# Kernel tuning notes

Hardware: AMD Instinct MI355X
Metric: run time of the kernel (lower is better)

## Reference

```python
import jax, jax.numpy as jnp
import numpy as np

V, E, H = 50000, 300, 512
T, BIO, BIO_E = 9, 10, 64
REL_E, R = 128, 50
B, L = 16, 128


def _lstm(x, wih, whh, bih, bhh):
    # x: [B, L, E]; PyTorch gate order i, f, g, o
    h0 = jnp.zeros((x.shape[0], whh.shape[1]), x.dtype)
    def step(carry, xt):
        h, c = carry
        g = xt @ wih.T + h @ whh.T + (bih + bhh)
        i, f, gg, o = jnp.split(g, 4, axis=-1)
        c = jax.nn.sigmoid(f) * c + jax.nn.sigmoid(i) * jnp.tanh(gg)
        h = jax.nn.sigmoid(o) * jnp.tanh(c)
        return (h, c), h
    _, hs = jax.lax.scan(step, (h0, h0), jnp.swapaxes(x, 0, 1))
    return jnp.swapaxes(hs, 0, 1)


def _crf_nll(emi, tags, mask, trans, start, end):
    # torchcrf-style linear-chain CRF NLL, mean reduction. emi: [B,L,T]
    mf = mask.astype(emi.dtype)
    ar = jnp.arange(emi.shape[0])
    emi_t = jnp.swapaxes(emi, 0, 1)   # [L,B,T]
    tags_t = jnp.swapaxes(tags, 0, 1)
    mf_t = jnp.swapaxes(mf, 0, 1)
    num0 = start[tags_t[0]] + emi_t[0][ar, tags_t[0]]
    def num_step(carry, inp):
        prev, score = carry
        e_t, t_t, m_t = inp
        score = score + (trans[prev, t_t] + e_t[ar, t_t]) * m_t
        prev = jnp.where(m_t > 0, t_t, prev)
        return (prev, score), None
    (last, num), _ = jax.lax.scan(num_step, (tags_t[0], num0), (emi_t[1:], tags_t[1:], mf_t[1:]))
    num = num + end[last]
    def den_step(alpha, inp):
        e_t, m_t = inp
        nxt = jax.nn.logsumexp(alpha[:, :, None] + trans[None] + e_t[:, None, :], axis=1)
        return jnp.where(m_t[:, None] > 0, nxt, alpha), None
    alpha, _ = jax.lax.scan(den_step, start[None] + emi_t[0], (emi_t[1:], mf_t[1:]))
    den = jax.nn.logsumexp(alpha + end[None], axis=1)
    return -jnp.mean(num - den)


def setup_inputs() -> dict:
    key = jax.random.key(0)
    ks = jax.random.split(key, 24)
    lengths = jax.random.randint(ks[0], (B,), L // 2, L + 1)
    tok = jax.random.randint(ks[1], (B, L), 1, V)
    tokens = jnp.where(jnp.arange(L)[None, :] < lengths[:, None], tok, 0)  # 0 = <pad>
    n = lambda k, shp, s=0.05: jax.random.normal(k, shp, dtype=jnp.float32) * s
    z = lambda shp: jnp.zeros(shp, jnp.float32)
    return dict(
        tokens=tokens,
        bio_gold=jax.random.randint(ks[2], (B, L), 0, T),
        selection_gold=jax.random.randint(ks[3], (B, L, R, L), 0, 2).astype(jnp.int32),
        is_train=1,
        word_emb=n(ks[4], (V, E), 0.02),
        rel_emb=n(ks[5], (R, REL_E), 0.1),
        bio_emb=n(ks[6], (BIO, BIO_E), 0.1),
        w_ih_f=n(ks[7], (4 * H, E)), w_hh_f=n(ks[8], (4 * H, H)),
        b_ih_f=n(ks[9], (4 * H,)), b_hh_f=n(ks[10], (4 * H,)),
        w_ih_b=n(ks[11], (4 * H, E)), w_hh_b=n(ks[12], (4 * H, H)),
        b_ih_b=n(ks[13], (4 * H,)), b_hh_b=n(ks[14], (4 * H,)),
        emission_w=n(ks[15], (T, H)), emission_b=z((T,)),
        sel_u_w=n(ks[16], (REL_E, H + BIO_E)), sel_u_b=z((REL_E,)),
        sel_v_w=n(ks[17], (REL_E, H + BIO_E)), sel_v_b=z((REL_E,)),
        sel_uv_w=n(ks[18], (REL_E, 2 * REL_E)), sel_uv_b=z((REL_E,)),
        crf_trans=n(ks[19], (T, T), 0.1),
        crf_start=n(ks[20], (T,), 0.1),
        crf_end=n(ks[21], (T,), 0.1),
    )


def reference(tokens, bio_gold, selection_gold, is_train, word_emb, rel_emb, bio_emb,
              w_ih_f, w_hh_f, b_ih_f, b_hh_f, w_ih_b, w_hh_b, b_ih_b, b_hh_b,
              emission_w, emission_b, sel_u_w, sel_u_b, sel_v_w, sel_v_b,
              sel_uv_w, sel_uv_b, crf_trans, crf_start, crf_end):
    mask = tokens != 0
    emb = word_emb[tokens]                                 # [B,L,E]
    hf = _lstm(emb, w_ih_f, w_hh_f, b_ih_f, b_hh_f)
    hb = _lstm(emb[:, ::-1], w_ih_b, w_hh_b, b_ih_b, b_hh_b)[:, ::-1]
    o = (hf + hb) * 0.5                                    # avg of the two directions
    emi = o @ emission_w.T + emission_b                    # [B,L,T]
    crf_loss = _crf_nll(emi, bio_gold, mask, crf_trans, crf_start, crf_end)
    oc = jnp.concatenate([o, bio_emb[bio_gold]], axis=-1)  # [B,L,H+BIO_E]
    u = jax.nn.relu(oc @ sel_u_w.T + sel_u_b)              # [B,L,REL_E]
    v = jax.nn.relu(oc @ sel_v_w.T + sel_v_b)
    # linear(concat(u_j, v_i)) == u_j @ W1.T + v_i @ W2.T  (fused, avoids [B,L,L,2R])
    w1, w2 = sel_uv_w[:, :REL_E], sel_uv_w[:, REL_E:]
    uv = jax.nn.relu((u @ w1.T)[:, None, :, :] + (v @ w2.T)[:, :, None, :] + sel_uv_b)  # [B,L,L,REL_E]
    logits = jnp.einsum('bijh,rh->birj', uv, rel_emb)      # [B,L,R,L]
    g = selection_gold.astype(logits.dtype)
    bce = jnp.maximum(logits, 0) - logits * g + jnp.log1p(jnp.exp(-jnp.abs(logits)))
    pm = (mask[:, :, None] & mask[:, None, :])[:, :, None, :].astype(logits.dtype)
    sel_loss = jnp.sum(bce * pm) / jnp.sum(mask).astype(logits.dtype)
    return crf_loss + sel_loss
```

## Files before the change

kernel.cpp:

```cpp
#include <hip/hip_runtime.h>
#include <math.h>

#define NB   16
#define SL   128
#define ED   300
#define HD   512
#define G4   2048
#define NT   9
#define BE   64
#define RE   128
#define NR   50
#define OCD  576
#define NTOK 2048

__device__ __forceinline__ float sigf(float x){ return 1.0f/(1.0f + __expf(-x)); }

template<int TM>
__device__ __forceinline__ void gemm_body(const float* __restrict__ A, int lda,
                                          const float* __restrict__ Bm, int ldb,
                                          float* __restrict__ C, int ldc,
                                          int N, int K,
                                          const float* __restrict__ bias1,
                                          const float* __restrict__ bias2,
                                          int do_relu, int m_blk, int n_blk)
// ... 53 lines not shown
                float4 a4 = *(const float4*)&As[k][tm + i*4];
                float am[4] = {a4.x, a4.y, a4.z, a4.w};
                #pragma unroll
                for (int mm = 0; mm < 4; ++mm){
                    #pragma unroll
                    for (int nn = 0; nn < 4; ++nn)
                        acc[i*4+mm][nn] += am[mm]*bn[nn];
                }
            }
        }
    }
    float bv[4];
    #pragma unroll
    for (int nn=0;nn<4;++nn){
        int gn = n_blk + tn + nn;
        float bb = 0.f;
        if (gn < N){
            if (bias1) bb += bias1[gn];
            if (bias2) bb += bias2[gn];
        }
        bv[nn] = bb;
    }
    bool vec = ((ldc & 3) == 0) && (n_blk + tn + 3 < N);
    #pragma unroll
    for (int mm = 0; mm < TR; ++mm){
        int gm = m_blk + tm + mm;
        float r0 = acc[mm][0] + bv[0];
        float r1 = acc[mm][1] + bv[1];
        float r2 = acc[mm][2] + bv[2];
        float r3 = acc[mm][3] + bv[3];
        if (do_relu){ r0=fmaxf(r0,0.f); r1=fmaxf(r1,0.f); r2=fmaxf(r2,0.f); r3=fmaxf(r3,0.f); }
        if (vec){
            *(float4*)(C + (size_t)gm*ldc + n_blk + tn) = make_float4(r0,r1,r2,r3);
        } else {
            int gn = n_blk + tn;
            if (gn   < N) C[(size_t)gm*ldc + gn  ] = r0;
            if (gn+1 < N) C[(size_t)gm*ldc + gn+1] = r1;
            if (gn+2 < N) C[(size_t)gm*ldc + gn+2] = r2;
            if (gn+3 < N) C[(size_t)gm*ldc + gn+3] = r3;
        }
    }
}

template<int TM>
__global__ __launch_bounds__(256) void gemm_k(const float* __restrict__ A, int lda,
                                              const float* __restrict__ Bm, int ldb,
                                              float* __restrict__ C, int ldc,
                                              int N, int K,
                                              const float* __restrict__ bias1,
                                              const float* __restrict__ bias2,
                                              int do_relu)
{
    gemm_body<TM>(A, lda, Bm, ldb, C, ldc, N, K, bias1, bias2, do_relu,
                  blockIdx.x * TM, blockIdx.y * 64);
}

template<int TM>
__global__ __launch_bounds__(256) void gemm_dual_k(const float* __restrict__ A0, const float* __restrict__ A1, int lda,
                                                   const float* __restrict__ B0, const float* __restrict__ B1, int ldb,
                                                   float* __restrict__ C0, float* __restrict__ C1, int ldc,
                                                   int N, int K,
                                                   const float* __restrict__ bias0, const float* __restrict__ bias1,
                                                   int do_relu)
{
    const int z = blockIdx.z;
    gemm_body<TM>(z ? A1 : A0, lda, z ? B1 : B0, ldb, z ? C1 : C0, ldc, N, K,
                  z ? bias1 : bias0, nullptr, do_relu, blockIdx.x * TM, blockIdx.y * 64);
}

__global__ __launch_bounds__(256) void gemm_emb_k(const int* __restrict__ tokens,
                                                  const float* __restrict__ word_emb,
                                                  const float* __restrict__ B0, const float* __restrict__ B1,
                                                  float* __restrict__ C0, float* __restrict__ C1,
                                                  const float* __restrict__ bi0a, const float* __restrict__ bi0b,
                                                  const float* __restrict__ bi1a, const float* __restrict__ bi1b)
{
    __shared__ float As[16][132];
    __shared__ float Bs[16][68];
    const int z = blockIdx.z;
    const float* Bm = z ? B1 : B0;
    float* C       = z ? C1 : C0;
    const float* ba = z ? bi1a : bi0a;
    const float* bb = z ? bi1b : bi0b;
    const int t = threadIdx.x;
    const int m_blk = blockIdx.x * 128;
    const int n_blk = blockIdx.y * 64;
    const int tm = (t >> 4) * 8;
    const int tn = (t & 15) * 4;
    float acc[8][4];
    #pragma unroll
    for (int i=0;i<8;++i){ acc[i][0]=0.f; acc[i][1]=0.f; acc[i][2]=0.f; acc[i][3]=0.f; }

    for (int ck = 0; ck < 19; ++ck){
        const int k0 = ck << 4;
        __syncthreads();
        #pragma unroll
        for (int it = 0; it < 2; ++it){
            int task = t + it*256;
            int m = task >> 2, q = task & 3;
            int kk = k0 + q*4;
            const int tok = tokens[m_blk + m];
            const float* ap = word_emb + (size_t)tok*ED + kk;
            float4 v = make_float4(0.f,0.f,0.f,0.f);
            if (kk + 3 < ED) v = *(const float4*)ap;
            else {
                if (kk   < ED) v.x = ap[0];
                if (kk+1 < ED) v.y = ap[1];
                if (kk+2 < ED) v.z = ap[2];
            }
            As[q*4+0][m] = v.x; As[q*4+1][m] = v.y; As[q*4+2][m] = v.z; As[q*4+3][m] = v.w;
        }
        {
            int n = t >> 2, q = t & 3;
            int kk = k0 + q*4;
            const float* bp = Bm + (size_t)(n_blk + n)*ED + kk;
            float4 v = make_float4(0.f,0.f,0.f,0.f);
            if (kk + 3 < ED) v = *(const float4*)bp;
            else {
                if (kk   < ED) v.x = bp[0];
                if (kk+1 < ED) v.y = bp[1];
                if (kk+2 < ED) v.z = bp[2];
            }
            Bs[q*4+0][n] = v.x; Bs[q*4+1][n] = v.y; Bs[q*4+2][n] = v.z; Bs[q*4+3][n] = v.w;
        }
        __syncthreads();
        #pragma unroll
        for (int k = 0; k < 16; ++k){
            float4 b4 = *(const float4*)&Bs[k][tn];
            float bn[4] = {b4.x, b4.y, b4.z, b4.w};
            #pragma unroll
            for (int i = 0; i < 2; ++i){
                float4 a4 = *(const float4*)&As[k][tm + i*4];
                float am[4] = {a4.x, a4.y, a4.z, a4.w};
                #pragma unroll
                for (int mm = 0; mm < 4; ++mm){
                    #pragma unroll
                    for (int nn = 0; nn < 4; ++nn)
                        acc[i*4+mm][nn] += am[mm]*bn[nn];
                }
            }
        }
    }
    float bv[4];
    #pragma unroll
    for (int nn=0;nn<4;++nn){ int gn = n_blk + tn + nn; bv[nn] = ba[gn] + bb[gn]; }
    #pragma unroll
    for (int mm = 0; mm < 8; ++mm){
        int gm = m_blk + tm + mm;
        *(float4*)(C + (size_t)gm*G4 + n_blk + tn) =
            make_float4(acc[mm][0]+bv[0], acc[mm][1]+bv[1], acc[mm][2]+bv[2], acc[mm][3]+bv[3]);
    }
}

__global__ __launch_bounds__(256, 1) void lstm_k(const float* __restrict__ xwf,
                                                 const float* __restrict__ xwb,
                                                 const float* __restrict__ whhf,
                                                 const float* __restrict__ whhb,
                                                 unsigned long long* __restrict__ hteam,
                                                 float* __restrict__ hf_all,
                                                 float* __restrict__ hb_all)
{
    __shared__ __align__(16) float h_sf[2*HD];
    __shared__ __align__(16) float h_sb[2*HD];
    __shared__ __align__(16) float part[8*128];
    __shared__ float gates_s[128];
    __shared__ float cst[64];
    const int wg   = blockIdx.x;
    const int team = wg >> 5;
    const int rank = wg & 31;
    const int b0   = team * 2;
    const int t    = threadIdx.x;
    const int wv   = t >> 6;
    const int lane = t & 63;
    const int rg   = t & 31;
    const int kc   = t >> 5;
    const int lr0  = rg*2, lr1 = rg*2 + 1;
    const int grow0 = (lr0 >> 4)*HD + rank*16 + (lr0 & 15);
    const int grow1 = (lr1 >> 4)*HD + rank*16 + (lr1 & 15);
    unsigned long long* hTf = hteam + (size_t)(team*2 + 0)*2*1024;
    unsigned long long* hTb = hteam + (size_t)(team*2 + 1)*2*1024;

    float4 wf0[16], wf1[16], wb0[16], wb1[16];
    {
        const float* p0 = whhf + (size_t)grow0*HD + kc*64;
        const float* p1 = whhf + (size_t)grow1*HD + kc*64;
        const float* p2 = whhb + (size_t)grow0*HD + kc*64;
        const float* p3 = whhb + (size_t)grow1*HD + kc*64;
        #pragma unroll
        for (int q = 0; q < 16; ++q){
            wf0[q] = *(const float4*)(p0 + q*4);
            wf1[q] = *(const float4*)(p1 + q*4);
            wb0[q] = *(const float4*)(p2 + q*4);
            wb1[q] = *(const float4*)(p3 + q*4);
        }
    }
    const int rrow = t >> 1, rb2 = t & 1;
    const int growr = (rrow >> 4)*HD + rank*16 + (rrow & 15);
    const int ahl = t >> 1, ab2 = t & 1;
    const int hidx_a = rank*16 + ahl;
    const int s0 = wv*128 + lane;

    if (t < 64) cst[t] = 0.f;
    __syncthreads();

    int par = 0;
    for (int s = 0; s < SL; ++s){
        float xval_f = 0.f, xval_b = 0.f;
        if (t < 128){
            xval_f = xwf[(size_t)((b0 + rb2)*SL + s)*G4 + growr];
            xval_b = xwb[(size_t)((b0 + rb2)*SL + (SL-1 - s))*G4 + growr];
        }
        {
            const unsigned long long* src = hTf + (size_t)par*1024;
            unsigned long long v0,v1,v2,v3;
            const unsigned want = (unsigned)s;
            for (;;){
                v0 = __hip_atomic_load(&src[      s0     ], __ATOMIC_RELAXED, __HIP_MEMORY_SCOPE_AGENT);
                v1 = __hip_atomic_load(&src[      s0 + 64], __ATOMIC_RELAXED, __HIP_MEMORY_SCOPE_AGENT);
                v2 = __hip_atomic_load(&src[512 + s0     ], __ATOMIC_RELAXED, __HIP_MEMORY_SCOPE_AGENT);
                v3 = __hip_atomic_load(&src[512 + s0 + 64], __ATOMIC_RELAXED, __HIP_MEMORY_SCOPE_AGENT);
                if (((unsigned)(v0>>32)==want) & ((unsigned)(v1>>32)==want) &
                    ((unsigned)(v2>>32)==want) & ((unsigned)(v3>>32)==want)) break;
                __builtin_amdgcn_s_sleep(1);
            }
            h_sf[     s0     ] = __uint_as_float((unsigned)v0);
            h_sf[     s0 + 64] = __uint_as_float((unsigned)v1);
            h_sf[HD + s0     ] = __uint_as_float((unsigned)v2);
            h_sf[HD + s0 + 64] = __uint_as_float((unsigned)v3);
        }
        const unsigned long long* srcb = hTb + (size_t)par*1024;
        unsigned long long p0 = __hip_atomic_load(&srcb[      s0     ], __ATOMIC_RELAXED, __HIP_MEMORY_SCOPE_AGENT);
        unsigned long long p1 = __hip_atomic_load(&srcb[      s0 + 64], __ATOMIC_RELAXED, __HIP_MEMORY_SCOPE_AGENT);
        unsigned long long p2 = __hip_atomic_load(&srcb[512 + s0     ], __ATOMIC_RELAXED, __HIP_MEMORY_SCOPE_AGENT);
        unsigned long long p3 = __hip_atomic_load(&srcb[512 + s0 + 64], __ATOMIC_RELAXED, __HIP_MEMORY_SCOPE_AGENT);
        {
            float a00=0.f,a01=0.f,a10=0.f,a11=0.f;
            #pragma unroll
            for (int q = 0; q < 16; ++q){
                float4 wa = wf0[q], wb = wf1[q];
                float4 h0 = *(const float4*)(h_sf + 0*HD + kc*64 + q*4);
                float4 h1 = *(const float4*)(h_sf + 1*HD + kc*64 + q*4);
                a00 += wa.x*h0.x + wa.y*h0.y + wa.z*h0.z + wa.w*h0.w;
                a01 += wa.x*h1.x + wa.y*h1.y + wa.z*h1.z + wa.w*h1.w;
                a10 += wb.x*h0.x + wb.y*h0.y + wb.z*h0.z + wb.w*h0.w;
                a11 += wb.x*h1.x + wb.y*h1.y + wb.z*h1.z + wb.w*h1.w;
            }
            *(float4*)&part[kc*128 + lr0*2] = make_float4(a00,a01,a10,a11);
        }
        __syncthreads();
        if (t < 128){
            float g = 0.f;
            #pragma unroll
            for (int c = 0; c < 8; ++c) g += part[c*128 + t];
            gates_s[t] = g + xval_f;
        }
        __syncthreads();
        if (t < 32){
            float gi = gates_s[(0*16 + ahl)*2 + ab2];
            float gf = gates_s[(1*16 + ahl)*2 + ab2];
            float gc = gates_s[(2*16 + ahl)*2 + ab2];
            float go_ = gates_s[(3*16 + ahl)*2 + ab2];
            float cp = cst[t];
            float cn = sigf(gf)*cp + sigf(gi)*tanhf(gc);
            float hn = sigf(go_)*tanhf(cn);
            cst[t] = cn;
            unsigned long long pk = ((unsigned long long)(unsigned)(s+1) << 32)
                                  | (unsigned long long)__float_as_uint(hn);
            __hip_atomic_store(&hTf[(size_t)(par^1)*1024 + ab2*512 + hidx_a], pk,
                               __ATOMIC_RELAXED, __HIP_MEMORY_SCOPE_AGENT);
            hf_all[(size_t)((b0 + ab2)*SL + s)*HD + hidx_a] = hn;
        }
        {
            const unsigned want = (unsigned)s;
            if (!(((unsigned)(p0>>32)==want) & ((unsigned)(p1>>32)==want) &
                  ((unsigned)(p2>>32)==want) & ((unsigned)(p3>>32)==want))){
                for (;;){
                    p0 = __hip_atomic_load(&srcb[      s0     ], __ATOMIC_RELAXED, __HIP_MEMORY_SCOPE_AGENT);
                    p1 = __hip_atomic_load(&srcb[      s0 + 64], __ATOMIC_RELAXED, __HIP_MEMORY_SCOPE_AGENT);
                    p2 = __hip_atomic_load(&srcb[512 + s0     ], __ATOMIC_RELAXED, __HIP_MEMORY_SCOPE_AGENT);
                    p3 = __hip_atomic_load(&srcb[512 + s0 + 64], __ATOMIC_RELAXED, __HIP_MEMORY_SCOPE_AGENT);
                    if (((unsigned)(p0>>32)==want) & ((unsigned)(p1>>32)==want) &
                        ((unsigned)(p2>>32)==want) & ((unsigned)(p3>>32)==want)) break;
                    __builtin_amdgcn_s_sleep(1);
                }
            }
            h_sb[     s0     ] = __uint_as_float((unsigned)p0);
            h_sb[     s0 + 64] = __uint_as_float((unsigned)p1);
            h_sb[HD + s0     ] = __uint_as_float((unsigned)p2);
            h_sb[HD + s0 + 64] = __uint_as_float((unsigned)p3);
        }
        {
            float a00=0.f,a01=0.f,a10=0.f,a11=0.f;
            #pragma unroll
            for (int q = 0; q < 16; ++q){
                float4 wa = wb0[q], wb = wb1[q];
                float4 h0 = *(const float4*)(h_sb + 0*HD + kc*64 + q*4);
                float4 h1 = *(const float4*)(h_sb + 1*HD + kc*64 + q*4);
                a00 += wa.x*h0.x + wa.y*h0.y + wa.z*h0.z + wa.w*h0.w;
                a01 += wa.x*h1.x + wa.y*h1.y + wa.z*h1.z + wa.w*h1.w;
                a10 += wb.x*h0.x + wb.y*h0.y + wb.z*h0.z + wb.w*h0.w;
                a11 += wb.x*h1.x + wb.y*h1.y + wb.z*h1.z + wb.w*h1.w;
            }
            *(float4*)&part[kc*128 + lr0*2] = make_float4(a00,a01,a10,a11);
        }
        __syncthreads();
        if (t < 128){
            float g = 0.f;
            #pragma unroll
            for (int c = 0; c < 8; ++c) g += part[c*128 + t];
            gates_s[t] = g + xval_b;
        }
        __syncthreads();
        if (t < 32){
            float gi = gates_s[(0*16 + ahl)*2 + ab2];
            float gf = gates_s[(1*16 + ahl)*2 + ab2];
            float gc = gates_s[(2*16 + ahl)*2 + ab2];
            float go_ = gates_s[(3*16 + ahl)*2 + ab2];
            float cp = cst[32 + t];
            float cn = sigf(gf)*cp + sigf(gi)*tanhf(gc);
            float hn = sigf(go_)*tanhf(cn);
            cst[32 + t] = cn;
            unsigned long long pk = ((unsigned long long)(unsigned)(s+1) << 32)
                                  | (unsigned long long)__float_as_uint(hn);
            __hip_atomic_store(&hTb[(size_t)(par^1)*1024 + ab2*512 + hidx_a], pk,
                               __ATOMIC_RELAXED, __HIP_MEMORY_SCOPE_AGENT);
            hb_all[(size_t)((b0 + ab2)*SL + (SL-1 - s))*HD + hidx_a] = hn;
        }
        par ^= 1;
    }
}

__global__ __launch_bounds__(256) void combine_k(const float* __restrict__ hf,
                                                 const float* __restrict__ hb,
                                                 const int* __restrict__ bio_gold,
                                                 const float* __restrict__ bio_emb,
                                                 float* __restrict__ oc)
{
    int idx = blockIdx.x*256 + threadIdx.x;
    if (idx >= NTOK*144) return;
    int row = idx / 144;
    int c4 = (idx - row*144) * 4;
    float4 v;
    if (c4 < HD){
        float4 a = *(const float4*)(hf + (size_t)row*HD + c4);
        float4 b = *(const float4*)(hb + (size_t)row*HD + c4);
        v = make_float4(0.5f*(a.x+b.x), 0.5f*(a.y+b.y), 0.5f*(a.z+b.z), 0.5f*(a.w+b.w));
    } else {
        int bg = bio_gold[row];
        v = *(const float4*)(bio_emb + bg*BE + (c4 - HD));
    }
    *(float4*)(oc + (size_t)row*OCD + c4) = v;
}

__global__ __launch_bounds__(64) void crf_k(const float* __restrict__ emi,
                                            const int* __restrict__ tags,
                                            const int* __restrict__ tokens,
                                            const float* __restrict__ trans,
                                            const float* __restrict__ startv,
                                            const float* __restrict__ endv,
                                            float* __restrict__ out_crf,
                                            float* __restrict__ out_m)
{
    const int b = blockIdx.x, lane = threadIdx.x;
    unsigned long long m0 = __ballot(tokens[b*SL + lane] != 0);
    unsigned long long m1 = __ballot(tokens[b*SL + 64 + lane] != 0);
    const int len = __popcll(m0) + __popcll(m1);
    float npart = 0.f;
    #pragma unroll
    for (int half = 0; half < 2; ++half){
        int tt = lane + half*64;
        if (tt >= 1 && tt < len){
            int tp = tags[b*SL + tt - 1], tc = tags[b*SL + tt];
            npart += trans[tp*NT + tc] + emi[(size_t)(b*SL + tt)*NT + tc];
        }
    }
    #pragma unroll
    for (int off = 32; off > 0; off >>= 1) npart += __shfl_down(npart, off);
    float tr[NT]; float alpha = -1e30f;
    if (lane < NT){
        #pragma unroll
        for (int i = 0; i < NT; ++i) tr[i] = trans[i*NT + lane];
        alpha = startv[lane] + emi[(size_t)(b*SL)*NT + lane];
    }
    for (int tt = 1; tt < SL; ++tt){
        float al[NT];
        #pragma unroll
        for (int i = 0; i < NT; ++i) al[i] = __shfl(alpha, i);
        if (lane < NT && tt < len){
            float mx = -1e30f;
            #pragma unroll
            for (int i = 0; i < NT; ++i) mx = fmaxf(mx, al[i] + tr[i]);
            float se = 0.f;
            #pragma unroll
            for (int i = 0; i < NT; ++i) se += __expf(al[i] + tr[i] - mx);
            alpha = mx + __logf(se) + emi[(size_t)(b*SL + tt)*NT + lane];
        }
    }
    float alf = (lane < NT) ? (alpha + endv[lane]) : -1e30f;
    float alE[NT];
    #pragma unroll
    for (int i = 0; i < NT; ++i) alE[i] = __shfl(alf, i);
    if (lane == 0){
        float mx = -1e30f;
        #pragma unroll
        for (int i = 0; i < NT; ++i) mx = fmaxf(mx, alE[i]);
        float se = 0.f;
        #pragma unroll
        for (int i = 0; i < NT; ++i) se += __expf(alE[i] - mx);
        float den = mx + __logf(se);
        int t0g = tags[b*SL];
        float num = startv[t0g] + emi[(size_t)(b*SL)*NT + t0g] + npart;
        num += endv[tags[b*SL + len - 1]];
        atomicAdd(out_crf, -(num - den) * (1.0f/16.0f));
        atomicAdd(out_m, (float)len);
    }
}

__global__ __launch_bounds__(256) void sel_k(const float* __restrict__ U2,
                                             const float* __restrict__ V2,
                                             const float* __restrict__ uvb,
                                             const float* __restrict__ rel_emb,
                                             const int* __restrict__ gold,
                                             const int* __restrict__ tokens,
                                             float* __restrict__ out_sel)
{
    __shared__ float ret_s[RE][52];
    __shared__ float pt_s[RE][68];
    __shared__ float vb_s[RE];
    __shared__ float mk_s[64];
    __shared__ float red_s[4];
    const int jt = blockIdx.x, qi = blockIdx.y, b = blockIdx.z;
    const int t = threadIdx.x;
    if (tokens[b*SL + qi] == 0) return;
    if (t < 32){
        float4 v4 = *(const float4*)(V2 + (size_t)(b*SL + qi)*RE + t*4);
        float4 b4 = *(const float4*)(uvb + t*4);
        vb_s[t*4+0] = v4.x + b4.x; vb_s[t*4+1] = v4.y + b4.y;
        vb_s[t*4+2] = v4.z + b4.z; vb_s[t*4+3] = v4.w + b4.w;
    }
    if (t < 64) mk_s[t] = (tokens[b*SL + jt*64 + t] != 0) ? 1.f : 0.f;
    {
        int r = t & 63;
        for (int q = t >> 6; q < 32; q += 4){
            if (r < NR){
                float4 e4 = *(const float4*)(rel_emb + (size_t)r*RE + q*4);
                ret_s[q*4+0][r] = e4.x; ret_s[q*4+1][r] = e4.y;
                ret_s[q*4+2][r] = e4.z; ret_s[q*4+3][r] = e4.w;
            } else if (r < 64){
                ret_s[q*4+0][r] = 0.f; ret_s[q*4+1][r] = 0.f;
                ret_s[q*4+2][r] = 0.f; ret_s[q*4+3][r] = 0.f;
            }
        }
    }
    __syncthreads();
    {
        int j = t & 63;
        for (int q = t >> 6; q < 32; q += 4){
            float4 u4 = *(const float4*)(U2 + (size_t)(b*SL + jt*64 + j)*RE + q*4);
            pt_s[q*4+0][j] = fmaxf(u4.x + vb_s[q*4+0], 0.f);
            pt_s[q*4+1][j] = fmaxf(u4.y + vb_s[q*4+1], 0.f);
            pt_s[q*4+2][j] = fmaxf(u4.z + vb_s[q*4+2], 0.f);
            pt_s[q*4+3][j] = fmaxf(u4.w + vb_s[q*4+3], 0.f);
        }
    }
    __syncthreads();
    const int mj = (t & 15) * 4;
    const int nr = (t >> 4) * 4;
    float accv[4][4];
    #pragma unroll
    for (int i=0;i<4;++i){ accv[i][0]=0.f; accv[i][1]=0.f; accv[i][2]=0.f; accv[i][3]=0.f; }
    #pragma unroll 4
    for (int k = 0; k < RE; ++k){
        float4 aj = *(const float4*)&pt_s[k][mj];
        float4 br = *(const float4*)&ret_s[k][nr];
        float am[4] = {aj.x, aj.y, aj.z, aj.w};
        float bn[4] = {br.x, br.y, br.z, br.w};
        #pragma unroll
        for (int mm = 0; mm < 4; ++mm){
            #pragma unroll
            for (int nn = 0; nn < 4; ++nn)
                accv[mm][nn] += am[mm]*bn[nn];
        }
    }
    float lsum = 0.f;
    #pragma unroll
    for (int nn = 0; nn < 4; ++nn){
        int r = nr + nn;
        if (r < NR){
            const int* gp = gold + (size_t)((b*SL + qi)*NR + r)*SL + jt*64 + mj;
            #pragma unroll
            for (int mm = 0; mm < 4; ++mm){
                float l = accv[mm][nn];
                float g = (float)gp[mm];
                float bce = fmaxf(l, 0.f) - l*g + __logf(1.f + __expf(-fabsf(l)));
                lsum += bce * mk_s[mj + mm];
            }
        }
    }
    #pragma unroll
    for (int off = 32; off > 0; off >>= 1) lsum += __shfl_down(lsum, off);
    if ((t & 63) == 0) red_s[t >> 6] = lsum;
    __syncthreads();
    if (t == 0) atomicAdd(out_sel, red_s[0]+red_s[1]+red_s[2]+red_s[3]);
}

__global__ void finalize_k(const float* __restrict__ accum, float* __restrict__ out)
{
    if (threadIdx.x == 0 && blockIdx.x == 0) out[0] = accum[0] + accum[1] / accum[2];
}

extern "C" void kernel_launch(void* const* d_in, const int* in_sizes, int n_in,
                              void* d_out, int out_size, void* d_ws, size_t ws_size,
                              hipStream_t stream)
{
    const int*   tokens    = (const int*)  d_in[0];
    const int*   bio_gold  = (const int*)  d_in[1];
    const int*   sel_gold  = (const int*)  d_in[2];
    const float* word_emb  = (const float*)d_in[4];
    const float* rel_emb   = (const float*)d_in[5];
    const float* bio_emb   = (const float*)d_in[6];
    const float* w_ih_f    = (const float*)d_in[7];
    const float* w_hh_f    = (const float*)d_in[8];
    const float* b_ih_f    = (const float*)d_in[9];
    const float* b_hh_f    = (const float*)d_in[10];
    const float* w_ih_b    = (const float*)d_in[11];
    const float* w_hh_b    = (const float*)d_in[12];
    const float* b_ih_b    = (const float*)d_in[13];
    const float* b_hh_b    = (const float*)d_in[14];
    const float* emission_w= (const float*)d_in[15];
    const float* emission_b= (const float*)d_in[16];
    const float* sel_u_w   = (const float*)d_in[17];
    const float* sel_u_b   = (const float*)d_in[18];
    const float* sel_v_w   = (const float*)d_in[19];
    const float* sel_v_b   = (const float*)d_in[20];
    const float* sel_uv_w  = (const float*)d_in[21];
    const float* sel_uv_b  = (const float*)d_in[22];
    const float* crf_trans = (const float*)d_in[23];
    const float* crf_start = (const float*)d_in[24];
    const float* crf_end   = (const float*)d_in[25];
    (void)in_sizes; (void)n_in; (void)out_size; (void)ws_size;

    float* ws     = (float*)d_ws;
    float* emb    = ws;
    float* xwf    = emb    + (size_t)NTOK*ED;
    float* xwb    = xwf    + (size_t)NTOK*G4;
    float* hf_all = xwb    + (size_t)NTOK*G4;
    float* hb_all = hf_all + (size_t)NTOK*HD;
    float* oc     = hb_all + (size_t)NTOK*HD;
    float* emi    = oc     + (size_t)NTOK*OCD;
    float* u_     = emi    + (size_t)NTOK*NT;
    float* v_     = u_     + (size_t)NTOK*RE;
    float* U2     = v_     + (size_t)NTOK*RE;
    float* V2     = U2     + (size_t)NTOK*RE;
    float* accum  = V2     + (size_t)NTOK*RE;

    unsigned long long* hteam = (unsigned long long*)emb;

    hipMemsetAsync(accum, 0, 4*sizeof(float), stream);
    hipMemsetAsync(hteam, 0, (size_t)8*2*2*1024*sizeof(unsigned long long), stream);

    gemm_emb_k<<<dim3(NTOK/128, G4/64, 2), 256, 0, stream>>>(tokens, word_emb,
                                                             w_ih_f, w_ih_b, xwf, xwb,
                                                             b_ih_f, b_hh_f, b_ih_b, b_hh_b);

    {
        const float *p_xwf = xwf, *p_xwb = xwb, *p_whf = w_hh_f, *p_whb = w_hh_b;
        unsigned long long* p_ht = hteam;
        float *p_hf = hf_all, *p_hb = hb_all;
        void* args[7] = {&p_xwf, &p_xwb, &p_whf, &p_whb, &p_ht, &p_hf, &p_hb};
        hipLaunchCooperativeKernel(lstm_k, dim3(256), dim3(256), args, 0u, stream);
    }

    combine_k<<<(NTOK*144 + 255)/256, 256, 0, stream>>>(hf_all, hb_all, bio_gold, bio_emb, oc);

    gemm_k<64><<<dim3(NTOK/64, 1), 256, 0, stream>>>(oc, OCD, emission_w, HD, emi, NT, NT, HD, emission_b, nullptr, 0);
    gemm_dual_k<64><<<dim3(NTOK/64, 2, 2), 256, 0, stream>>>(oc, oc, OCD, sel_u_w, sel_v_w, OCD,
                                                             u_, v_, RE, RE, OCD, sel_u_b, sel_v_b, 1);
    gemm_dual_k<64><<<dim3(NTOK/64, 2, 2), 256, 0, stream>>>(u_, v_, RE, sel_uv_w, sel_uv_w + RE, 2*RE,
                                                             U2, V2, RE, RE, RE, nullptr, nullptr, 0);

    crf_k<<<NB, 64, 0, stream>>>(emi, bio_gold, tokens, crf_trans, crf_start, crf_end, accum + 0, accum + 2);
    sel_k<<<dim3(2, SL, NB), 256, 0, stream>>>(U2, V2, sel_uv_b, rel_emb, sel_gold, tokens, accum + 1);

    finalize_k<<<1, 1, 0, stream>>>(accum, (float*)d_out);
}
```

Measured before the change: 991.2 us.

## Interleave four batch-pair recurrences per workgroup team, halving LSTM grid

```diff
diff --git a/kernel.cpp b/kernel.cpp
--- a/kernel.cpp
+++ b/kernel.cpp
@@ -229,6 +229,18 @@
     }
 }
 
+__device__ __forceinline__ unsigned long long agld(const unsigned long long* p){
+    return __hip_atomic_load(p, __ATOMIC_RELAXED, __HIP_MEMORY_SCOPE_AGENT);
+}
+__device__ __forceinline__ void agst(unsigned long long* p, unsigned long long v){
+    __hip_atomic_store(p, v, __ATOMIC_RELAXED, __HIP_MEMORY_SCOPE_AGENT);
+}
+__device__ __forceinline__ bool tagok(unsigned long long a, unsigned long long b,
+                                      unsigned long long c, unsigned long long d, unsigned w){
+    return ((unsigned)(a>>32)==w) & ((unsigned)(b>>32)==w) &
+           ((unsigned)(c>>32)==w) & ((unsigned)(d>>32)==w);
+}
+
 __global__ __launch_bounds__(256, 1) void lstm_k(const float* __restrict__ xwf,
                                                  const float* __restrict__ xwb,
                                                  const float* __restrict__ whhf,
@@ -237,15 +249,14 @@
                                                  float* __restrict__ hf_all,
                                                  float* __restrict__ hb_all)
 {
-    __shared__ __align__(16) float h_sf[2*HD];
-    __shared__ __align__(16) float h_sb[2*HD];
+    __shared__ __align__(16) float h_s[4][2*HD];
     __shared__ __align__(16) float part[8*128];
     __shared__ float gates_s[128];
-    __shared__ float cst[64];
+    __shared__ float cst[4*32];
     const int wg   = blockIdx.x;
     const int team = wg >> 5;
     const int rank = wg & 31;
-    const int b0   = team * 2;
+    const int b0   = team * 4;
     const int t    = threadIdx.x;
     const int wv   = t >> 6;
     const int lane = t & 63;
@@ -254,8 +265,10 @@
     const int lr0  = rg*2, lr1 = rg*2 + 1;
     const int grow0 = (lr0 >> 4)*HD + rank*16 + (lr0 & 15);
     const int grow1 = (lr1 >> 4)*HD + rank*16 + (lr1 & 15);
-    unsigned long long* hTf = hteam + (size_t)(team*2 + 0)*2*1024;
-    unsigned long long* hTb = hteam + (size_t)(team*2 + 1)*2*1024;
+    unsigned long long* hT0 = hteam + (size_t)((team*4 + 0)*2)*1024;
+    unsigned long long* hT1 = hteam + (size_t)((team*4 + 1)*2)*1024;
+    unsigned long long* hT2 = hteam + (size_t)((team*4 + 2)*2)*1024;
+    unsigned long long* hT3 = hteam + (size_t)((team*4 + 3)*2)*1024;
 
     float4 wf0[16], wf1[16], wb0[16], wb1[16];
     {
@@ -277,46 +290,54 @@
     const int hidx_a = rank*16 + ahl;
     const int s0 = wv*128 + lane;
 
-    if (t < 64) cst[t] = 0.f;
+    if (t < 128) cst[t] = 0.f;
     __syncthreads();
+
+    unsigned long long c0a, c0b, c0c, c0d;
+    {
+        const unsigned long long* src = hT0;
+        c0a = agld(&src[s0]); c0b = agld(&src[s0+64]);
+        c0c = agld(&src[512+s0]); c0d = agld(&src[512+s0+64]);
+    }
 
     int par = 0;
     for (int s = 0; s < SL; ++s){
-        float xval_f = 0.f, xval_b = 0.f;
+        const unsigned want = (unsigned)s;
+        const unsigned long long tag1 = ((unsigned long long)(unsigned)(s+1)) << 32;
+        float xv0 = 0.f, xv1 = 0.f, xv2 = 0.f, xv3 = 0.f;
         if (t < 128){
-            xval_f = xwf[(size_t)((b0 + rb2)*SL + s)*G4 + growr];
-            xval_b = xwb[(size_t)((b0 + rb2)*SL + (SL-1 - s))*G4 + growr];
-        }
-        {
-            const unsigned long long* src = hTf + (size_t)par*1024;
-            unsigned long long v0,v1,v2,v3;
-            const unsigned want = (unsigned)s;
+            xv0 = xwf[(size_t)((b0     + rb2)*SL + s       )*G4 + growr];
+            xv1 = xwb[(size_t)((b0     + rb2)*SL + (SL-1-s))*G4 + growr];
+            xv2 = xwf[(size_t)((b0 + 2 + rb2)*SL + s       )*G4 + growr];
+            xv3 = xwb[(size_t)((b0 + 2 + rb2)*SL + (SL-1-s))*G4 + growr];
+        }
+
+        if (!tagok(c0a,c0b,c0c,c0d,want)){
+            const unsigned long long* src = hT0 + (size_t)par*1024;
             for (;;){
-                v0 = __hip_atomic_load(&src[      s0     ], __ATOMIC_RELAXED, __HIP_MEMORY_SCOPE_AGENT);
-                v1 = __hip_atomic_load(&src[      s0 + 64], __ATOMIC_RELAXED, __HIP_MEMORY_SCOPE_AGENT);
-                v2 = __hip_atomic_load(&src[512 + s0     ], __ATOMIC_RELAXED, __HIP_MEMORY_SCOPE_AGENT);
-                v3 = __hip_atomic_load(&src[512 + s0 + 64], __ATOMIC_RELAXED, __HIP_MEMORY_SCOPE_AGENT);
-                if (((unsigned)(v0>>32)==want) & ((unsigned)(v1>>32)==want) &
-                    ((unsigned)(v2>>32)==want) & ((unsigned)(v3>>32)==want)) break;
+                c0a = agld(&src[s0]); c0b = agld(&src[s0+64]);
+                c0c = agld(&src[512+s0]); c0d = agld(&src[512+s0+64]);
+                if (tagok(c0a,c0b,c0c,c0d,want)) break;
                 __builtin_amdgcn_s_sleep(1);
             }
-            h_sf[     s0     ] = __uint_as_float((unsigned)v0);
-            h_sf[     s0 + 64] = __uint_as_float((unsigned)v1);
-            h_sf[HD + s0     ] = __uint_as_float((unsigned)v2);
-            h_sf[HD + s0 + 64] = __uint_as_float((unsigned)v3);
-        }
-        const unsigned long long* srcb = hTb + (size_t)par*1024;
-        unsigned long long p0 = __hip_atomic_load(&srcb[      s0     ], __ATOMIC_RELAXED, __HIP_MEMORY_SCOPE_AGENT);
-        unsigned long long p1 = __hip_atomic_load(&srcb[      s0 + 64], __ATOMIC_RELAXED, __HIP_MEMORY_SCOPE_AGENT);
-        unsigned long long p2 = __hip_atomic_load(&srcb[512 + s0     ], __ATOMIC_RELAXED, __HIP_MEMORY_SCOPE_AGENT);
-        unsigned long long p3 = __hip_atomic_load(&srcb[512 + s0 + 64], __ATOMIC_RELAXED, __HIP_MEMORY_SCOPE_AGENT);
+        }
+        h_s[0][     s0     ] = __uint_as_float((unsigned)c0a);
+        h_s[0][     s0 + 64] = __uint_as_float((unsigned)c0b);
+        h_s[0][HD + s0     ] = __uint_as_float((unsigned)c0c);
+        h_s[0][HD + s0 + 64] = __uint_as_float((unsigned)c0d);
+        unsigned long long c1a, c1b, c1c, c1d;
+        {
+            const unsigned long long* src = hT1 + (size_t)par*1024;
+            c1a = agld(&src[s0]); c1b = agld(&src[s0+64]);
+            c1c = agld(&src[512+s0]); c1d = agld(&src[512+s0+64]);
+        }
         {
             float a00=0.f,a01=0.f,a10=0.f,a11=0.f;
             #pragma unroll
             for (int q = 0; q < 16; ++q){
                 float4 wa = wf0[q], wb = wf1[q];
-                float4 h0 = *(const float4*)(h_sf + 0*HD + kc*64 + q*4);
-                float4 h1 = *(const float4*)(h_sf + 1*HD + kc*64 + q*4);
+                float4 h0 = *(const float4*)(&h_s[0][0]  + kc*64 + q*4);
+                float4 h1 = *(const float4*)(&h_s[0][HD] + kc*64 + q*4);
                 a00 += wa.x*h0.x + wa.y*h0.y + wa.z*h0.z + wa.w*h0.w;
                 a01 += wa.x*h1.x + wa.y*h1.y + wa.z*h1.z + wa.w*h1.w;
                 a10 += wb.x*h0.x + wb.y*h0.y + wb.z*h0.z + wb.w*h0.w;
@@ -329,7 +350,7 @@
             float g = 0.f;
             #pragma unroll
             for (int c = 0; c < 8; ++c) g += part[c*128 + t];
-            gates_s[t] = g + xval_f;
+            gates_s[t] = g + xv0;
         }
         __syncthreads();
         if (t < 32){
@@ -341,38 +362,37 @@
             float cn = sigf(gf)*cp + sigf(gi)*tanhf(gc);
             float hn = sigf(go_)*tanhf(cn);
             cst[t] = cn;
-            unsigned long long pk = ((unsigned long long)(unsigned)(s+1) << 32)
-                                  | (unsigned long long)__float_as_uint(hn);
-            __hip_atomic_store(&hTf[(size_t)(par^1)*1024 + ab2*512 + hidx_a], pk,
-                               __ATOMIC_RELAXED, __HIP_MEMORY_SCOPE_AGENT);
+            agst(&hT0[(size_t)(par^1)*1024 + ab2*512 + hidx_a],
+                 tag1 | (unsigned long long)__float_as_uint(hn));
             hf_all[(size_t)((b0 + ab2)*SL + s)*HD + hidx_a] = hn;
         }
-        {
-            const unsigned want = (unsigned)s;
-            if (!(((unsigned)(p0>>32)==want) & ((unsigned)(p1>>32)==want) &
-                  ((unsigned)(p2>>32)==want) & ((unsigned)(p3>>32)==want))){
-                for (;;){
-                    p0 = __hip_atomic_load(&srcb[      s0     ], __ATOMIC_RELAXED, __HIP_MEMORY_SCOPE_AGENT);
-                    p1 = __hip_atomic_load(&srcb[      s0 + 64], __ATOMIC_RELAXED, __HIP_MEMORY_SCOPE_AGENT);
-                    p2 = __hip_atomic_load(&srcb[512 + s0     ], __ATOMIC_RELAXED, __HIP_MEMORY_SCOPE_AGENT);
-                    p3 = __hip_atomic_load(&srcb[512 + s0 + 64], __ATOMIC_RELAXED, __HIP_MEMORY_SCOPE_AGENT);
-                    if (((unsigned)(p0>>32)==want) & ((unsigned)(p1>>32)==want) &
-                        ((unsigned)(p2>>32)==want) & ((unsigned)(p3>>32)==want)) break;
-                    __builtin_amdgcn_s_sleep(1);
-                }
-            }
-            h_sb[     s0     ] = __uint_as_float((unsigned)p0);
-            h_sb[     s0 + 64] = __uint_as_float((unsigned)p1);
-            h_sb[HD + s0     ] = __uint_as_float((unsigned)p2);
-            h_sb[HD + s0 + 64] = __uint_as_float((unsigned)p3);
+
+        if (!tagok(c1a,c1b,c1c,c1d,want)){
+            const unsigned long long* src = hT1 + (size_t)par*1024;
+            for (;;){
+                c1a = agld(&src[s0]); c1b = agld(&src[s0+64]);
+                c1c = agld(&src[512+s0]); c1d = agld(&src[512+s0+64]);
+                if (tagok(c1a,c1b,c1c,c1d,want)) break;
+                __builtin_amdgcn_s_sleep(1);
+            }
+        }
+        h_s[1][     s0     ] = __uint_as_float((unsigned)c1a);
+        h_s[1][     s0 + 64] = __uint_as_float((unsigned)c1b);
+        h_s[1][HD + s0     ] = __uint_as_float((unsigned)c1c);
+        h_s[1][HD + s0 + 64] = __uint_as_float((unsigned)c1d);
+        unsigned long long c2a, c2b, c2c, c2d;
+        {
+            const unsigned long long* src = hT2 + (size_t)par*1024;
+            c2a = agld(&src[s0]); c2b = agld(&src[s0+64]);
+            c2c = agld(&src[512+s0]); c2d = agld(&src[512+s0+64]);
         }
         {
             float a00=0.f,a01=0.f,a10=0.f,a11=0.f;
             #pragma unroll
             for (int q = 0; q < 16; ++q){
                 float4 wa = wb0[q], wb = wb1[q];
-                float4 h0 = *(const float4*)(h_sb + 0*HD + kc*64 + q*4);
-                float4 h1 = *(const float4*)(h_sb + 1*HD + kc*64 + q*4);
+                float4 h0 = *(const float4*)(&h_s[1][0]  + kc*64 + q*4);
+                float4 h1 = *(const float4*)(&h_s[1][HD] + kc*64 + q*4);
                 a00 += wa.x*h0.x + wa.y*h0.y + wa.z*h0.z + wa.w*h0.w;
                 a01 += wa.x*h1.x + wa.y*h1.y + wa.z*h1.z + wa.w*h1.w;
                 a10 += wb.x*h0.x + wb.y*h0.y + wb.z*h0.z + wb.w*h0.w;
@@ -385,7 +405,7 @@
             float g = 0.f;
             #pragma unroll
             for (int c = 0; c < 8; ++c) g += part[c*128 + t];
-            gates_s[t] = g + xval_b;
+            gates_s[t] = g + xv1;
         }
         __syncthreads();
         if (t < 32){
@@ -397,11 +417,118 @@
             float cn = sigf(gf)*cp + sigf(gi)*tanhf(gc);
             float hn = sigf(go_)*tanhf(cn);
             cst[32 + t] = cn;
-            unsigned long long pk = ((unsigned long long)(unsigned)(s+1) << 32)
-                                  | (unsigned long long)__float_as_uint(hn);
-            __hip_atomic_store(&hTb[(size_t)(par^1)*1024 + ab2*512 + hidx_a], pk,
-                               __ATOMIC_RELAXED, __HIP_MEMORY_SCOPE_AGENT);
+            agst(&hT1[(size_t)(par^1)*1024 + ab2*512 + hidx_a],
+                 tag1 | (unsigned long long)__float_as_uint(hn));
             hb_all[(size_t)((b0 + ab2)*SL + (SL-1 - s))*HD + hidx_a] = hn;
+        }
+
+        if (!tagok(c2a,c2b,c2c,c2d,want)){
+            const unsigned long long* src = hT2 + (size_t)par*1024;
+            for (;;){
+                c2a = agld(&src[s0]); c2b = agld(&src[s0+64]);
+                c2c = agld(&src[512+s0]); c2d = agld(&src[512+s0+64]);
+                if (tagok(c2a,c2b,c2c,c2d,want)) break;
+                __builtin_amdgcn_s_sleep(1);
+            }
+        }
+        h_s[2][     s0     ] = __uint_as_float((unsigned)c2a);
+        h_s[2][     s0 + 64] = __uint_as_float((unsigned)c2b);
+        h_s[2][HD + s0     ] = __uint_as_float((unsigned)c2c);
+        h_s[2][HD + s0 + 64] = __uint_as_float((unsigned)c2d);
+        unsigned long long c3a, c3b, c3c, c3d;
+        {
+            const unsigned long long* src = hT3 + (size_t)par*1024;
+            c3a = agld(&src[s0]); c3b = agld(&src[s0+64]);
+            c3c = agld(&src[512+s0]); c3d = agld(&src[512+s0+64]);
+        }
+        {
+            float a00=0.f,a01=0.f,a10=0.f,a11=0.f;
+            #pragma unroll
+            for (int q = 0; q < 16; ++q){
+                float4 wa = wf0[q], wb = wf1[q];
+                float4 h0 = *(const float4*)(&h_s[2][0]  + kc*64 + q*4);
+                float4 h1 = *(const float4*)(&h_s[2][HD] + kc*64 + q*4);
+                a00 += wa.x*h0.x + wa.y*h0.y + wa.z*h0.z + wa.w*h0.w;
+                a01 += wa.x*h1.x + wa.y*h1.y + wa.z*h1.z + wa.w*h1.w;
+                a10 += wb.x*h0.x + wb.y*h0.y + wb.z*h0.z + wb.w*h0.w;
+                a11 += wb.x*h1.x + wb.y*h1.y + wb.z*h1.z + wb.w*h1.w;
+            }
+            *(float4*)&part[kc*128 + lr0*2] = make_float4(a00,a01,a10,a11);
+        }
+        __syncthreads();
+        if (t < 128){
+            float g = 0.f;
+            #pragma unroll
+            for (int c = 0; c < 8; ++c) g += part[c*128 + t];
+            gates_s[t] = g + xv2;
+        }
+        __syncthreads();
+        if (t < 32){
+            float gi = gates_s[(0*16 + ahl)*2 + ab2];
+            float gf = gates_s[(1*16 + ahl)*2 + ab2];
+            float gc = gates_s[(2*16 + ahl)*2 + ab2];
+            float go_ = gates_s[(3*16 + ahl)*2 + ab2];
+            float cp = cst[64 + t];
+            float cn = sigf(gf)*cp + sigf(gi)*tanhf(gc);
+            float hn = sigf(go_)*tanhf(cn);
+            cst[64 + t] = cn;
+            agst(&hT2[(size_t)(par^1)*1024 + ab2*512 + hidx_a],
+                 tag1 | (unsigned long long)__float_as_uint(hn));
+            hf_all[(size_t)((b0 + 2 + ab2)*SL + s)*HD + hidx_a] = hn;
+        }
+
+        if (!tagok(c3a,c3b,c3c,c3d,want)){
+            const unsigned long long* src = hT3 + (size_t)par*1024;
+            for (;;){
+                c3a = agld(&src[s0]); c3b = agld(&src[s0+64]);
+                c3c = agld(&src[512+s0]); c3d = agld(&src[512+s0+64]);
+                if (tagok(c3a,c3b,c3c,c3d,want)) break;
+                __builtin_amdgcn_s_sleep(1);
+            }
+        }
+        h_s[3][     s0     ] = __uint_as_float((unsigned)c3a);
+        h_s[3][     s0 + 64] = __uint_as_float((unsigned)c3b);
+        h_s[3][HD + s0     ] = __uint_as_float((unsigned)c3c);
+        h_s[3][HD + s0 + 64] = __uint_as_float((unsigned)c3d);
+        {
+            const unsigned long long* src = hT0 + (size_t)(par^1)*1024;
+            c0a = agld(&src[s0]); c0b = agld(&src[s0+64]);
+            c0c = agld(&src[512+s0]); c0d = agld(&src[512+s0+64]);
+        }
+        {
+            float a00=0.f,a01=0.f,a10=0.f,a11=0.f;
+            #pragma unroll
+            for (int q = 0; q < 16; ++q){
+                float4 wa = wb0[q], wb = wb1[q];
+                float4 h0 = *(const float4*)(&h_s[3][0]  + kc*64 + q*4);
+                float4 h1 = *(const float4*)(&h_s[3][HD] + kc*64 + q*4);
+                a00 += wa.x*h0.x + wa.y*h0.y + wa.z*h0.z + wa.w*h0.w;
+                a01 += wa.x*h1.x + wa.y*h1.y + wa.z*h1.z + wa.w*h1.w;
+                a10 += wb.x*h0.x + wb.y*h0.y + wb.z*h0.z + wb.w*h0.w;
+                a11 += wb.x*h1.x + wb.y*h1.y + wb.z*h1.z + wb.w*h1.w;
+            }
+            *(float4*)&part[kc*128 + lr0*2] = make_float4(a00,a01,a10,a11);
+        }
+        __syncthreads();
+        if (t < 128){
+            float g = 0.f;
+            #pragma unroll
+            for (int c = 0; c < 8; ++c) g += part[c*128 + t];
+            gates_s[t] = g + xv3;
+        }
+        __syncthreads();
+        if (t < 32){
+            float gi = gates_s[(0*16 + ahl)*2 + ab2];
+            float gf = gates_s[(1*16 + ahl)*2 + ab2];
+            float gc = gates_s[(2*16 + ahl)*2 + ab2];
+            float go_ = gates_s[(3*16 + ahl)*2 + ab2];
+            float cp = cst[96 + t];
+            float cn = sigf(gf)*cp + sigf(gi)*tanhf(gc);
+            float hn = sigf(go_)*tanhf(cn);
+            cst[96 + t] = cn;
+            agst(&hT3[(size_t)(par^1)*1024 + ab2*512 + hidx_a],
+                 tag1 | (unsigned long long)__float_as_uint(hn));
+            hb_all[(size_t)((b0 + 2 + ab2)*SL + (SL-1 - s))*HD + hidx_a] = hn;
         }
         par ^= 1;
     }
@@ -634,7 +761,7 @@
     unsigned long long* hteam = (unsigned long long*)emb;
 
     hipMemsetAsync(accum, 0, 4*sizeof(float), stream);
-    hipMemsetAsync(hteam, 0, (size_t)8*2*2*1024*sizeof(unsigned long long), stream);
+    hipMemsetAsync(hteam, 0, (size_t)4*4*2*1024*sizeof(unsigned long long), stream);
 
     gemm_emb_k<<<dim3(NTOK/128, G4/64, 2), 256, 0, stream>>>(tokens, word_emb,
                                                              w_ih_f, w_ih_b, xwf, xwb,
@@ -645,7 +772,7 @@
         unsigned long long* p_ht = hteam;
         float *p_hf = hf_all, *p_hb = hb_all;
         void* args[7] = {&p_xwf, &p_xwb, &p_whf, &p_whb, &p_ht, &p_hf, &p_hb};
-        hipLaunchCooperativeKernel(lstm_k, dim3(256), dim3(256), args, 0u, stream);
+        hipLaunchCooperativeKernel(lstm_k, dim3(128), dim3(256), args, 0u, stream);
     }
 
     combine_k<<<(NTOK*144 + 255)/256, 256, 0, stream>>>(hf_all, hb_all, bio_gold, bio_emb, oc);
```

After: 1.435 ms. 44.7% more time.

## Split LSTM forward and backward directions into separate workgroups

Applied to the files above, without the earlier changes.

```diff
diff --git a/kernel.cpp b/kernel.cpp
--- a/kernel.cpp
+++ b/kernel.cpp
@@ -229,7 +229,19 @@
     }
 }
 
-__global__ __launch_bounds__(256, 1) void lstm_k(const float* __restrict__ xwf,
+__device__ __forceinline__ unsigned long long agld(const unsigned long long* p){
+    return __hip_atomic_load(p, __ATOMIC_RELAXED, __HIP_MEMORY_SCOPE_AGENT);
+}
+__device__ __forceinline__ void agst(unsigned long long* p, unsigned long long v){
+    __hip_atomic_store(p, v, __ATOMIC_RELAXED, __HIP_MEMORY_SCOPE_AGENT);
+}
+__device__ __forceinline__ bool tagok(unsigned long long a, unsigned long long b,
+                                      unsigned long long c, unsigned long long d, unsigned w){
+    return ((unsigned)(a>>32)==w) & ((unsigned)(b>>32)==w) &
+           ((unsigned)(c>>32)==w) & ((unsigned)(d>>32)==w);
+}
+
+__global__ __launch_bounds__(256, 2) void lstm_k(const float* __restrict__ xwf,
                                                  const float* __restrict__ xwb,
                                                  const float* __restrict__ whhf,
                                                  const float* __restrict__ whhb,
@@ -237,14 +249,15 @@
                                                  float* __restrict__ hf_all,
                                                  float* __restrict__ hb_all)
 {
-    __shared__ __align__(16) float h_sf[2*HD];
-    __shared__ __align__(16) float h_sb[2*HD];
+    __shared__ __align__(16) float h_s[2*HD];
     __shared__ __align__(16) float part[8*128];
     __shared__ float gates_s[128];
-    __shared__ float cst[64];
+    __shared__ float cst[32];
     const int wg   = blockIdx.x;
-    const int team = wg >> 5;
-    const int rank = wg & 31;
+    const int dir  = wg >> 8;
+    const int id8  = wg & 255;
+    const int team = id8 >> 5;
+    const int rank = id8 & 31;
     const int b0   = team * 2;
     const int t    = threadIdx.x;
     const int wv   = t >> 6;
@@ -254,21 +267,19 @@
     const int lr0  = rg*2, lr1 = rg*2 + 1;
     const int grow0 = (lr0 >> 4)*HD + rank*16 + (lr0 & 15);
     const int grow1 = (lr1 >> 4)*HD + rank*16 + (lr1 & 15);
-    unsigned long long* hTf = hteam + (size_t)(team*2 + 0)*2*1024;
-    unsigned long long* hTb = hteam + (size_t)(team*2 + 1)*2*1024;
-
-    float4 wf0[16], wf1[16], wb0[16], wb1[16];
+    const float* xw   = dir ? xwb    : xwf;
+    const float* whh  = dir ? whhb   : whhf;
+    float*       hall = dir ? hb_all : hf_all;
+    unsigned long long* hT = hteam + (size_t)((team*2 + dir)*2)*1024;
+
+    float4 w0[16], w1[16];
     {
-        const float* p0 = whhf + (size_t)grow0*HD + kc*64;
-        const float* p1 = whhf + (size_t)grow1*HD + kc*64;
-        const float* p2 = whhb + (size_t)grow0*HD + kc*64;
-        const float* p3 = whhb + (size_t)grow1*HD + kc*64;
+        const float* p0 = whh + (size_t)grow0*HD + kc*64;
+        const float* p1 = whh + (size_t)grow1*HD + kc*64;
         #pragma unroll
         for (int q = 0; q < 16; ++q){
-            wf0[q] = *(const float4*)(p0 + q*4);
-            wf1[q] = *(const float4*)(p1 + q*4);
-            wb0[q] = *(const float4*)(p2 + q*4);
-            wb1[q] = *(const float4*)(p3 + q*4);
+            w0[q] = *(const float4*)(p0 + q*4);
+            w1[q] = *(const float4*)(p1 + q*4);
         }
     }
     const int rrow = t >> 1, rb2 = t & 1;
@@ -277,46 +288,39 @@
     const int hidx_a = rank*16 + ahl;
     const int s0 = wv*128 + lane;
 
-    if (t < 64) cst[t] = 0.f;
+    if (t < 32) cst[t] = 0.f;
     __syncthreads();
 
     int par = 0;
     for (int s = 0; s < SL; ++s){
-        float xval_f = 0.f, xval_b = 0.f;
-        if (t < 128){
-            xval_f = xwf[(size_t)((b0 + rb2)*SL + s)*G4 + growr];
-            xval_b = xwb[(size_t)((b0 + rb2)*SL + (SL-1 - s))*G4 + growr];
-        }
+        const unsigned want = (unsigned)s;
+        const int sx = dir ? (SL-1 - s) : s;
+        float xval = 0.f;
+        if (t < 128)
+            xval = xw[(size_t)((b0 + rb2)*SL + sx)*G4 + growr];
         {
-            const unsigned long long* src = hTf + (size_t)par*1024;
-            unsigned long long v0,v1,v2,v3;
-            const unsigned want = (unsigned)s;
+            const unsigned long long* src = hT + (size_t)par*1024;
+            unsigned long long v0, v1, v2, v3;
             for (;;){
-                v0 = __hip_atomic_load(&src[      s0     ], __ATOMIC_RELAXED, __HIP_MEMORY_SCOPE_AGENT);
-                v1 = __hip_atomic_load(&src[      s0 + 64], __ATOMIC_RELAXED, __HIP_MEMORY_SCOPE_AGENT);
-                v2 = __hip_atomic_load(&src[512 + s0     ], __ATOMIC_RELAXED, __HIP_MEMORY_SCOPE_AGENT);
-                v3 = __hip_atomic_load(&src[512 + s0 + 64], __ATOMIC_RELAXED, __HIP_MEMORY_SCOPE_AGENT);
-                if (((unsigned)(v0>>32)==want) & ((unsigned)(v1>>32)==want) &
-                    ((unsigned)(v2>>32)==want) & ((unsigned)(v3>>32)==want)) break;
+                v0 = agld(&src[      s0     ]);
+                v1 = agld(&src[      s0 + 64]);
+                v2 = agld(&src[512 + s0     ]);
+                v3 = agld(&src[512 + s0 + 64]);
+                if (tagok(v0,v1,v2,v3,want)) break;
                 __builtin_amdgcn_s_sleep(1);
             }
-            h_sf[     s0     ] = __uint_as_float((unsigned)v0);
-            h_sf[     s0 + 64] = __uint_as_float((unsigned)v1);
-            h_sf[HD + s0     ] = __uint_as_float((unsigned)v2);
-            h_sf[HD + s0 + 64] = __uint_as_float((unsigned)v3);
-        }
-        const unsigned long long* srcb = hTb + (size_t)par*1024;
-        unsigned long long p0 = __hip_atomic_load(&srcb[      s0     ], __ATOMIC_RELAXED, __HIP_MEMORY_SCOPE_AGENT);
-        unsigned long long p1 = __hip_atomic_load(&srcb[      s0 + 64], __ATOMIC_RELAXED, __HIP_MEMORY_SCOPE_AGENT);
-        unsigned long long p2 = __hip_atomic_load(&srcb[512 + s0     ], __ATOMIC_RELAXED, __HIP_MEMORY_SCOPE_AGENT);
-        unsigned long long p3 = __hip_atomic_load(&srcb[512 + s0 + 64], __ATOMIC_RELAXED, __HIP_MEMORY_SCOPE_AGENT);
+            h_s[     s0     ] = __uint_as_float((unsigned)v0);
+            h_s[     s0 + 64] = __uint_as_float((unsigned)v1);
+            h_s[HD + s0     ] = __uint_as_float((unsigned)v2);
+            h_s[HD + s0 + 64] = __uint_as_float((unsigned)v3);
+        }
         {
             float a00=0.f,a01=0.f,a10=0.f,a11=0.f;
             #pragma unroll
             for (int q = 0; q < 16; ++q){
-                float4 wa = wf0[q], wb = wf1[q];
-                float4 h0 = *(const float4*)(h_sf + 0*HD + kc*64 + q*4);
-                float4 h1 = *(const float4*)(h_sf + 1*HD + kc*64 + q*4);
+                float4 wa = w0[q], wb = w1[q];
+                float4 h0 = *(const float4*)(h_s + 0*HD + kc*64 + q*4);
+                float4 h1 = *(const float4*)(h_s + 1*HD + kc*64 + q*4);
                 a00 += wa.x*h0.x + wa.y*h0.y + wa.z*h0.z + wa.w*h0.w;
                 a01 += wa.x*h1.x + wa.y*h1.y + wa.z*h1.z + wa.w*h1.w;
                 a10 += wb.x*h0.x + wb.y*h0.y + wb.z*h0.z + wb.w*h0.w;
@@ -329,13 +333,13 @@
             float g = 0.f;
             #pragma unroll
             for (int c = 0; c < 8; ++c) g += part[c*128 + t];
-            gates_s[t] = g + xval_f;
+            gates_s[t] = g + xval;
         }
         __syncthreads();
         if (t < 32){
-            float gi = gates_s[(0*16 + ahl)*2 + ab2];
-            float gf = gates_s[(1*16 + ahl)*2 + ab2];
-            float gc = gates_s[(2*16 + ahl)*2 + ab2];
+            float gi  = gates_s[(0*16 + ahl)*2 + ab2];
+            float gf  = gates_s[(1*16 + ahl)*2 + ab2];
+            float gc  = gates_s[(2*16 + ahl)*2 + ab2];
             float go_ = gates_s[(3*16 + ahl)*2 + ab2];
             float cp = cst[t];
             float cn = sigf(gf)*cp + sigf(gi)*tanhf(gc);
@@ -343,65 +347,8 @@
             cst[t] = cn;
             unsigned long long pk = ((unsigned long long)(unsigned)(s+1) << 32)
                                   | (unsigned long long)__float_as_uint(hn);
-            __hip_atomic_store(&hTf[(size_t)(par^1)*1024 + ab2*512 + hidx_a], pk,
-                               __ATOMIC_RELAXED, __HIP_MEMORY_SCOPE_AGENT);
-            hf_all[(size_t)((b0 + ab2)*SL + s)*HD + hidx_a] = hn;
-        }
-        {
-            const unsigned want = (unsigned)s;
-            if (!(((unsigned)(p0>>32)==want) & ((unsigned)(p1>>32)==want) &
-                  ((unsigned)(p2>>32)==want) & ((unsigned)(p3>>32)==want))){
-                for (;;){
-                    p0 = __hip_atomic_load(&srcb[      s0     ], __ATOMIC_RELAXED, __HIP_MEMORY_SCOPE_AGENT);
-                    p1 = __hip_atomic_load(&srcb[      s0 + 64], __ATOMIC_RELAXED, __HIP_MEMORY_SCOPE_AGENT);
-                    p2 = __hip_atomic_load(&srcb[512 + s0     ], __ATOMIC_RELAXED, __HIP_MEMORY_SCOPE_AGENT);
-                    p3 = __hip_atomic_load(&srcb[512 + s0 + 64], __ATOMIC_RELAXED, __HIP_MEMORY_SCOPE_AGENT);
-                    if (((unsigned)(p0>>32)==want) & ((unsigned)(p1>>32)==want) &
-                        ((unsigned)(p2>>32)==want) & ((unsigned)(p3>>32)==want)) break;
-                    __builtin_amdgcn_s_sleep(1);
-                }
-            }
-            h_sb[     s0     ] = __uint_as_float((unsigned)p0);
-            h_sb[     s0 + 64] = __uint_as_float((unsigned)p1);
-            h_sb[HD + s0     ] = __uint_as_float((unsigned)p2);
-            h_sb[HD + s0 + 64] = __uint_as_float((unsigned)p3);
-        }
-        {
-            float a00=0.f,a01=0.f,a10=0.f,a11=0.f;
-            #pragma unroll
-            for (int q = 0; q < 16; ++q){
-                float4 wa = wb0[q], wb = wb1[q];
-                float4 h0 = *(const float4*)(h_sb + 0*HD + kc*64 + q*4);
-                float4 h1 = *(const float4*)(h_sb + 1*HD + kc*64 + q*4);
-                a00 += wa.x*h0.x + wa.y*h0.y + wa.z*h0.z + wa.w*h0.w;
-                a01 += wa.x*h1.x + wa.y*h1.y + wa.z*h1.z + wa.w*h1.w;
-                a10 += wb.x*h0.x + wb.y*h0.y + wb.z*h0.z + wb.w*h0.w;
-                a11 += wb.x*h1.x + wb.y*h1.y + wb.z*h1.z + wb.w*h1.w;
-            }
-            *(float4*)&part[kc*128 + lr0*2] = make_float4(a00,a01,a10,a11);
-        }
-        __syncthreads();
-        if (t < 128){
-            float g = 0.f;
-            #pragma unroll
-            for (int c = 0; c < 8; ++c) g += part[c*128 + t];
-            gates_s[t] = g + xval_b;
-        }
-        __syncthreads();
-        if (t < 32){
-            float gi = gates_s[(0*16 + ahl)*2 + ab2];
-            float gf = gates_s[(1*16 + ahl)*2 + ab2];
-            float gc = gates_s[(2*16 + ahl)*2 + ab2];
-            float go_ = gates_s[(3*16 + ahl)*2 + ab2];
-            float cp = cst[32 + t];
-            float cn = sigf(gf)*cp + sigf(gi)*tanhf(gc);
-            float hn = sigf(go_)*tanhf(cn);
-            cst[32 + t] = cn;
-            unsigned long long pk = ((unsigned long long)(unsigned)(s+1) << 32)
-                                  | (unsigned long long)__float_as_uint(hn);
-            __hip_atomic_store(&hTb[(size_t)(par^1)*1024 + ab2*512 + hidx_a], pk,
-                               __ATOMIC_RELAXED, __HIP_MEMORY_SCOPE_AGENT);
-            hb_all[(size_t)((b0 + ab2)*SL + (SL-1 - s))*HD + hidx_a] = hn;
+            agst(&hT[(size_t)(par^1)*1024 + ab2*512 + hidx_a], pk);
+            hall[(size_t)((b0 + ab2)*SL + sx)*HD + hidx_a] = hn;
         }
         par ^= 1;
     }
@@ -645,7 +592,7 @@
         unsigned long long* p_ht = hteam;
         float *p_hf = hf_all, *p_hb = hb_all;
         void* args[7] = {&p_xwf, &p_xwb, &p_whf, &p_whb, &p_ht, &p_hf, &p_hb};
-        hipLaunchCooperativeKernel(lstm_k, dim3(256), dim3(256), args, 0u, stream);
+        hipLaunchCooperativeKernel(lstm_k, dim3(512), dim3(256), args, 0u, stream);
     }
 
     combine_k<<<(NTOK*144 + 255)/256, 256, 0, stream>>>(hf_all, hb_all, bio_gold, bio_emb, oc);
```

Result: faster. 865.3 us (-12.7%).
